# Kernel optimization log

Hardware: AMD Instinct MI355X
Metric: run time of the kernel (lower is better)

The kernel has to match this reference:

```python
import jax, jax.numpy as jnp
import numpy as np

B, N = 8, 6                 # batch, cameras
D, C = 45, 64               # depth bins, context channels
FH, FW = 8, 22              # feature-map height/width
GX, GY, GZ = 64, 64, 32     # BEV grid: W, H, D in the torch code
RES = 0.5
XOFF, YOFF, ZOFF = 16.0, 16.0, 8.0


def _frustum():
    # matches LSS.create_frustum: pixel coords over full 352x128 image, depths 1..45
    xs = jnp.linspace(0.0, 351.0, FW)
    ys = jnp.linspace(0.0, 127.0, FH)
    ds = jnp.arange(1.0, 46.0, 1.0)
    d, y, x = jnp.meshgrid(ds, ys, xs, indexing='ij')   # [D, FH, FW]
    return jnp.stack([x * d, y * d, d], axis=-1)         # [D, FH, FW, 3]


def setup_inputs() -> dict:
    key = jax.random.key(0)
    k1, k2, k3 = jax.random.split(key, 3)
    # depthNet output: softmax over depth bins
    depth = jax.nn.softmax(jax.random.normal(k1, (B, N, D, FH, FW), dtype=jnp.float32), axis=2)
    feature = jax.random.normal(k2, (B, N, C, FH, FW), dtype=jnp.float32)
    # realistic pinhole intrinsics (invertible), identity rotations, small translations
    K = jnp.array([[250.0, 0.0, 176.0], [0.0, 250.0, 64.0], [0.0, 0.0, 1.0]], dtype=jnp.float32)
    intrinsics = jnp.tile(K, (B, N, 1, 1))
    rots = jnp.tile(jnp.eye(3, dtype=jnp.float32), (B, N, 1, 1))
    trans = jax.random.normal(k3, (B, N, 3), dtype=jnp.float32) * 0.5
    return {"depth": depth, "feature": feature, "rots": rots, "trans": trans, "intrinsics": intrinsics}


def reference(depth, feature, rots, trans, intrinsics):
    fr = _frustum()                                              # [D, FH, FW, 3]
    # get_geometry: unproject frustum to world
    inv_K = jnp.linalg.inv(intrinsics)                           # [B, N, 3, 3]
    pts_c = jnp.einsum('bnij,dhwj->bndhwi', inv_K, fr)           # camera frame
    geom = jnp.einsum('bnij,bndhwj->bndhwi', rots, pts_c) + trans[:, :, None, None, None, :]

    # context = depth outer-product feature: [B, N, D, C, FH, FW] -> [B,N,D,FH,FW,C]
    ctx = (depth[:, :, :, None] * feature[:, :, None]).transpose(0, 1, 2, 4, 5, 3)
    ctx = ctx.reshape(-1, C)                                     # [P, C]
    g = geom.reshape(-1, 3)                                      # [P, 3]

    # voxel index compute (astype int truncates toward zero, matching torch .long())
    nx = ((g[:, 0] + XOFF) / RES).astype(jnp.int32)
    ny = ((g[:, 2] + YOFF) / RES).astype(jnp.int32)
    nz = ((g[:, 1] + ZOFF) / RES).astype(jnp.int32)
    valid = (nx >= 0) & (nx < GX) & (ny >= 0) & (ny < GY) & (nz >= 0) & (nz < GZ)

    bidx = jnp.repeat(jnp.arange(B, dtype=jnp.int32), N * D * FH * FW)
    idx = jnp.where(valid, bidx * (GX * GY * GZ) + nx * (GY * GZ) + ny * GZ + nz, 0)

    # scatter-sum into dense BEV grid; invalid points contribute zero
    bev = jnp.zeros((B * GX * GY * GZ, C), dtype=ctx.dtype)
    bev = bev.at[idx].add(ctx * valid[:, None].astype(ctx.dtype))
    # [B, GX, GY, GZ, C] -> [B, C, GZ, GX, GY]
    return bev.reshape(B, GX, GY, GZ, C).transpose(0, 4, 3, 1, 2)
```

## Files before the change

### kernel.cpp

```cpp
#include <hip/hip_runtime.h>

#define BB 8
#define NN 6
#define DD 45
#define CC 64
#define FHH 8
#define FWW 22
#define GXX 64
#define GYY 64
#define GZZ 32
#define NPOINTS (BB*NN*DD*FHH*FWW)
#define NSITES (BB*NN*FHH*FWW)
#define ROWS (BB*GZZ)
#define NBINS (GXX*GYY)
#define CAPR 8192
#define HWSZ (FHH*FWW)

typedef float f32x4 __attribute__((ext_vector_type(4)));

#define WS_HIST_OFF 0
#define WS_OFF_OFF  ((size_t)ROWS * NBINS * 4)
#define WS_REC_OFF  (WS_OFF_OFF + (size_t)ROWS * 4097 * 4)
#define WS_SORT_OFF (WS_REC_OFF + (size_t)NPOINTS * 4)
#define WS_FEATG_OFF (WS_SORT_OFF + (size_t)ROWS * CAPR * 8)
#define WS_CNTR_OFF (WS_FEATG_OFF + (size_t)16 * NSITES * 16)
#define WS_NEEDED (WS_CNTR_OFF + (size_t)ROWS * 4)

__device__ __forceinline__ bool geom(int p, int& row, int& nxny,
                                     const float* __restrict__ rots,
                                     const float* __restrict__ trans,
                                     const float* __restrict__ intr)
{
    int w = p % FWW;
    int t = p / FWW;
    int h = t % FHH; t /= FHH;
    int di = t % DD; t /= DD;
    int n = t % NN;
    int b = t / NN;

    float d = (float)(di + 1);
    float x = (float)(351.0 * (double)w / 21.0);
    float y = (float)(127.0 * (double)h / 7.0);

    const float* K = intr + (b * NN + n) * 9;
    double k00 = K[0], k01 = K[1], k02 = K[2];
    double k10 = K[3], k11 = K[4], k12 = K[5];
    double k20 = K[6], k21 = K[7], k22 = K[8];
    double det = k00 * (k11 * k22 - k12 * k21)
               - k01 * (k10 * k22 - k12 * k20)
               + k02 * (k10 * k21 - k11 * k20);
    double id = 1.0 / det;
    float i00 = (float)(( k11 * k22 - k12 * k21) * id);
    float i01 = (float)((-k01 * k22 + k02 * k21) * id);
    float i02 = (float)(( k01 * k12 - k02 * k11) * id);
    float i10 = (float)((-k10 * k22 + k12 * k20) * id);
    float i11 = (float)(( k00 * k22 - k02 * k20) * id);
    float i12 = (float)((-k00 * k12 + k02 * k10) * id);
    float i20 = (float)(( k10 * k21 - k11 * k20) * id);
    float i21 = (float)((-k00 * k21 + k01 * k20) * id);
    float i22 = (float)(( k00 * k11 - k01 * k10) * id);

    float p0 = x * d, p1 = y * d, p2 = d;
    float c0 = i00 * p0 + i01 * p1 + i02 * p2;
    float c1 = i10 * p0 + i11 * p1 + i12 * p2;
    float c2 = i20 * p0 + i21 * p1 + i22 * p2;

    const float* R = rots + (b * NN + n) * 9;
    const float* T = trans + (b * NN + n) * 3;
    float g0 = R[0] * c0 + R[1] * c1 + R[2] * c2 + T[0];
    float g1 = R[3] * c0 + R[4] * c1 + R[5] * c2 + T[1];
    float g2 = R[6] * c0 + R[7] * c1 + R[8] * c2 + T[2];

    int nx = (int)((g0 + 16.0f) / 0.5f);
    int ny = (int)((g2 + 16.0f) / 0.5f);
    int nz = (int)((g1 + 8.0f)  / 0.5f);
    bool valid = (nx >= 0) & (nx < GXX) & (ny >= 0) & (ny < GYY) & (nz >= 0) & (nz < GZZ);

    row  = (b * GZZ + nz);
    nxny = (nx << 6) | ny;
    return valid;
}

__global__ __launch_bounds__(256) void lss_prep(const float* __restrict__ feature,
                                                int* __restrict__ hist,
                                                float4* __restrict__ featG) {
    int i = blockIdx.x * 256 + threadIdx.x;
    int stride = gridDim.x * 256;
    int4* h4 = (int4*)hist;
    int4 z4 = make_int4(0, 0, 0, 0);
    for (int k = i; k < ROWS * NBINS / 4; k += stride) h4[k] = z4;
    for (int k = i; k < 16 * NSITES; k += stride) {
        int site = k % NSITES;
        int ccb = k / NSITES;
        int hw = site % HWSZ;
        int cam = site / HWSZ;
        const float* fb = feature + ((size_t)cam * CC + ccb * 4) * HWSZ + hw;
        featG[k] = make_float4(fb[0], fb[HWSZ], fb[2 * HWSZ], fb[3 * HWSZ]);
    }
}

__global__ __launch_bounds__(256) void lss_build1(
    const float* __restrict__ rots, const float* __restrict__ trans,
    const float* __restrict__ intr,
    int* __restrict__ rec, int* __restrict__ hist)
{
    int p = blockIdx.x * 256 + threadIdx.x;
    int row, nxny;
    if (geom(p, row, nxny, rots, trans, intr)) {
        rec[p] = (row << 12) | nxny;
        atomicAdd(&hist[row * NBINS + nxny], 1);
    } else {
        rec[p] = -1;
    }
}

__global__ __launch_bounds__(256) void lss_scan(const int* __restrict__ hist,
                                                int* __restrict__ off,
                                                int* __restrict__ cnt_row) {
    int row = blockIdx.x;
    const int* h = hist + row * NBINS;
    int* o = off + row * 4097;
    int tid = threadIdx.x;

    int vals[16]; int sum = 0;
    #pragma unroll
    for (int i = 0; i < 16; ++i) { vals[i] = sum; sum += h[tid * 16 + i]; }

    __shared__ int ts[256];
    ts[tid] = sum;
    __syncthreads();
    for (int ofs = 1; ofs < 256; ofs <<= 1) {
        int v = (tid >= ofs) ? ts[tid - ofs] : 0;
        __syncthreads();
        ts[tid] += v;
        __syncthreads();
    }
    int base = tid ? ts[tid - 1] : 0;
    #pragma unroll
    for (int i = 0; i < 16; ++i)
        o[tid * 16 + i] = base + vals[i];
    if (tid == 255) { o[4096] = ts[255]; cnt_row[row] = ts[255]; }
}

__global__ __launch_bounds__(256) void lss_build2(
    const float* __restrict__ depth, const int* __restrict__ rec,
    int* __restrict__ off, int2* __restrict__ sorted)
{
    int p = blockIdx.x * 256 + threadIdx.x;
    int r = rec[p];
    if (r < 0) return;
    int row = r >> 12;
    int nxny = r & 4095;
    int w = p % FWW;
    int t = p / FWW;
    int h = t % FHH; t /= FHH;
    int cam = t / DD;
    int site = (cam * FHH + h) * FWW + w;
    float dv = depth[p];
    int pos = atomicAdd(&off[row * 4097 + nxny], 1);
    if (pos < CAPR)
        sorted[(size_t)row * CAPR + pos] = make_int2(__float_as_int(dv), (site << 12) | nxny);
}

__global__ __launch_bounds__(256) void lss_out8(
    const float4* __restrict__ featG,
    const int* __restrict__ cnt_row,
    const int2* __restrict__ sorted,
    float* __restrict__ out)
{
    int bid = blockIdx.x;
    int ccb = bid & 15;
    int row = bid >> 4;
    int b = row >> 5, nz = row & 31;
    int tid = threadIdx.x;

    int scnt = cnt_row[row];
    if (scnt > CAPR) scnt = CAPR;

    size_t ob0 = (((size_t)b * CC + ccb * 4) * GZZ + nz) * (GXX * GYY);
    const size_t cstride = (size_t)GZZ * GXX * GYY;

    if (scnt == 0) {
        f32x4 z = (f32x4){0.f, 0.f, 0.f, 0.f};
        #pragma unroll
        for (int cc = 0; cc < 4; ++cc) {
            f32x4* op = (f32x4*)(out + ob0 + (size_t)cc * cstride);
            #pragma unroll
            for (int k = 0; k < 4; ++k) op[tid + k * 256] = z;
        }
        return;
    }

    __shared__ float acc[4 * NBINS];
    {
        f32x4 z = (f32x4){0.f, 0.f, 0.f, 0.f};
        f32x4* a4 = (f32x4*)acc;
        #pragma unroll
        for (int k = 0; k < 16; ++k) a4[tid + k * 256] = z;
    }
    __syncthreads();

    const float4* fg = featG + (size_t)ccb * NSITES;
    const int2* bk = sorted + (size_t)row * CAPR;

    int E = (scnt + 255) >> 8;
    int s0 = tid * E;
    int e0 = s0 + E; if (e0 > scnt) e0 = scnt;

    f32x4 racc = (f32x4){0.f, 0.f, 0.f, 0.f};
    int rvox = -1;
    for (int e = s0; e < e0; ++e) {
        int2 en = bk[e];
        int meta = en.y;
        int vox = meta & 4095;
        float dv = __int_as_float(en.x);
        float4 f = fg[meta >> 12];
        if (vox != rvox) {
            if (rvox >= 0) {
                atomicAdd(&acc[0 * NBINS + rvox], racc.x);
                atomicAdd(&acc[1 * NBINS + rvox], racc.y);
                atomicAdd(&acc[2 * NBINS + rvox], racc.z);
                atomicAdd(&acc[3 * NBINS + rvox], racc.w);
            }
            rvox = vox;
            racc = (f32x4){0.f, 0.f, 0.f, 0.f};
        }
        racc.x += dv * f.x;
        racc.y += dv * f.y;
        racc.z += dv * f.z;
        racc.w += dv * f.w;
    }
    if (rvox >= 0) {
        atomicAdd(&acc[0 * NBINS + rvox], racc.x);
        atomicAdd(&acc[1 * NBINS + rvox], racc.y);
        atomicAdd(&acc[2 * NBINS + rvox], racc.z);
        atomicAdd(&acc[3 * NBINS + rvox], racc.w);
    }
    __syncthreads();

    #pragma unroll
    for (int cc = 0; cc < 4; ++cc) {
        const f32x4* a4 = (const f32x4*)(acc + cc * NBINS);
        f32x4* op = (f32x4*)(out + ob0 + (size_t)cc * cstride);
        for (int i = tid; i < 1024; i += 256)
            op[i] = a4[i];
    }
}

__global__ __launch_bounds__(256) void lss_zero(float4* __restrict__ p, int n4) {
    int i = blockIdx.x * blockDim.x + threadIdx.x;
    int stride = gridDim.x * blockDim.x;
    float4 z = make_float4(0.f, 0.f, 0.f, 0.f);
    for (; i < n4; i += stride) p[i] = z;
}

__global__ __launch_bounds__(256) void lss_scatter_direct(
    const float* __restrict__ depth, const float* __restrict__ feature,
    const float* __restrict__ rots, const float* __restrict__ trans,
    const float* __restrict__ intr, float* __restrict__ out)
{
    int p = blockIdx.x * 4 + (threadIdx.x >> 6);
    int lane = threadIdx.x & 63;
    int row, nxny;
    if (!geom(p, row, nxny, rots, trans, intr)) return;
    int b = row >> 5, nz = row & 31;
    int nx = nxny >> 6, ny = nxny & 63;
    int w = p % FWW;
    int t = p / FWW;
    int h = t % FHH; t /= FHH;
    int cam = t / DD;
    float dv = depth[p];
    float fv = feature[((size_t)cam * CC + lane) * HWSZ + h * FWW + w];
    size_t oidx = ((((size_t)b * CC + lane) * GZZ + nz) * GXX + nx) * GYY + ny;
    atomicAdd(out + oidx, dv * fv);
}

extern "C" void kernel_launch(void* const* d_in, const int* in_sizes, int n_in,
                              void* d_out, int out_size, void* d_ws, size_t ws_size,
                              hipStream_t stream) {
    const float* depth   = (const float*)d_in[0];
    const float* feature = (const float*)d_in[1];
    const float* rots    = (const float*)d_in[2];
    const float* trans   = (const float*)d_in[3];
    const float* intr    = (const float*)d_in[4];
    float* out = (float*)d_out;

    if (ws_size >= WS_NEEDED) {
        int*    hist    = (int*)((char*)d_ws + WS_HIST_OFF);
        int*    off     = (int*)((char*)d_ws + WS_OFF_OFF);
        int*    rec     = (int*)((char*)d_ws + WS_REC_OFF);
        int2*   sorted  = (int2*)((char*)d_ws + WS_SORT_OFF);
        float4* featG   = (float4*)((char*)d_ws + WS_FEATG_OFF);
        int*    cnt_row = (int*)((char*)d_ws + WS_CNTR_OFF);

        lss_prep<<<1024, 256, 0, stream>>>(feature, hist, featG);
        lss_build1<<<NPOINTS / 256, 256, 0, stream>>>(rots, trans, intr, rec, hist);
        lss_scan<<<ROWS, 256, 0, stream>>>(hist, off, cnt_row);
        lss_build2<<<NPOINTS / 256, 256, 0, stream>>>(depth, rec, off, sorted);
        lss_out8<<<ROWS * 16, 256, 0, stream>>>(featG, cnt_row, sorted, out);
    } else {
        lss_zero<<<4096, 256, 0, stream>>>((float4*)out, out_size / 4);
        lss_scatter_direct<<<NPOINTS / 4, 256, 0, stream>>>(depth, feature, rots, trans, intr, out);
    }
}
```

Measured before the change: 79.46 us.

## Split output accumulation to 2 channels per block and fold feature gather into scan

Result: no change. 78.62 us (-1.1%).

```diff
diff --git a/kernel.cpp b/kernel.cpp
--- a/kernel.cpp
+++ b/kernel.cpp
@@ -17,13 +17,14 @@
 #define HWSZ (FHH*FWW)
 
 typedef float f32x4 __attribute__((ext_vector_type(4)));
+typedef float f32x2 __attribute__((ext_vector_type(2)));
 
 #define WS_HIST_OFF 0
 #define WS_OFF_OFF  ((size_t)ROWS * NBINS * 4)
 #define WS_REC_OFF  (WS_OFF_OFF + (size_t)ROWS * 4097 * 4)
 #define WS_SORT_OFF (WS_REC_OFF + (size_t)NPOINTS * 4)
 #define WS_FEATG_OFF (WS_SORT_OFF + (size_t)ROWS * CAPR * 8)
-#define WS_CNTR_OFF (WS_FEATG_OFF + (size_t)16 * NSITES * 16)
+#define WS_CNTR_OFF (WS_FEATG_OFF + (size_t)32 * NSITES * 8)
 #define WS_NEEDED (WS_CNTR_OFF + (size_t)ROWS * 4)
 
 __device__ __forceinline__ bool geom(int p, int& row, int& nxny,
@@ -81,24 +82,6 @@
     return valid;
 }
 
-__global__ __launch_bounds__(256) void lss_prep(const float* __restrict__ feature,
-                                                int* __restrict__ hist,
-                                                float4* __restrict__ featG) {
-    int i = blockIdx.x * 256 + threadIdx.x;
-    int stride = gridDim.x * 256;
-    int4* h4 = (int4*)hist;
-    int4 z4 = make_int4(0, 0, 0, 0);
-    for (int k = i; k < ROWS * NBINS / 4; k += stride) h4[k] = z4;
-    for (int k = i; k < 16 * NSITES; k += stride) {
-        int site = k % NSITES;
-        int ccb = k / NSITES;
-        int hw = site % HWSZ;
-        int cam = site / HWSZ;
-        const float* fb = feature + ((size_t)cam * CC + ccb * 4) * HWSZ + hw;
-        featG[k] = make_float4(fb[0], fb[HWSZ], fb[2 * HWSZ], fb[3 * HWSZ]);
-    }
-}
-
 __global__ __launch_bounds__(256) void lss_build1(
     const float* __restrict__ rots, const float* __restrict__ trans,
     const float* __restrict__ intr,
@@ -116,7 +99,9 @@
 
 __global__ __launch_bounds__(256) void lss_scan(const int* __restrict__ hist,
                                                 int* __restrict__ off,
-                                                int* __restrict__ cnt_row) {
+                                                int* __restrict__ cnt_row,
+                                                const float* __restrict__ feature,
+                                                float2* __restrict__ featG2) {
     int row = blockIdx.x;
     const int* h = hist + row * NBINS;
     int* o = off + row * 4097;
@@ -140,6 +125,15 @@
     for (int i = 0; i < 16; ++i)
         o[tid * 16 + i] = base + vals[i];
     if (tid == 255) { o[4096] = ts[255]; cnt_row[row] = ts[255]; }
+
+    for (int k = blockIdx.x * 256 + tid; k < 32 * NSITES; k += ROWS * 256) {
+        int site = k % NSITES;
+        int ccp = k / NSITES;
+        int hw = site % HWSZ;
+        int cam = site / HWSZ;
+        const float* fb = feature + ((size_t)cam * CC + ccp * 2) * HWSZ + hw;
+        featG2[k] = make_float2(fb[0], fb[HWSZ]);
+    }
 }
 
 __global__ __launch_bounds__(256) void lss_build2(
@@ -162,28 +156,28 @@
         sorted[(size_t)row * CAPR + pos] = make_int2(__float_as_int(dv), (site << 12) | nxny);
 }
 
-__global__ __launch_bounds__(256) void lss_out8(
-    const float4* __restrict__ featG,
+__global__ __launch_bounds__(256) void lss_out9(
+    const float2* __restrict__ featG2,
     const int* __restrict__ cnt_row,
     const int2* __restrict__ sorted,
     float* __restrict__ out)
 {
     int bid = blockIdx.x;
-    int ccb = bid & 15;
-    int row = bid >> 4;
+    int ccp = bid & 31;
+    int row = bid >> 5;
     int b = row >> 5, nz = row & 31;
     int tid = threadIdx.x;
 
     int scnt = cnt_row[row];
     if (scnt > CAPR) scnt = CAPR;
 
-    size_t ob0 = (((size_t)b * CC + ccb * 4) * GZZ + nz) * (GXX * GYY);
+    size_t ob0 = (((size_t)b * CC + ccp * 2) * GZZ + nz) * (GXX * GYY);
     const size_t cstride = (size_t)GZZ * GXX * GYY;
 
     if (scnt == 0) {
         f32x4 z = (f32x4){0.f, 0.f, 0.f, 0.f};
         #pragma unroll
-        for (int cc = 0; cc < 4; ++cc) {
+        for (int cc = 0; cc < 2; ++cc) {
             f32x4* op = (f32x4*)(out + ob0 + (size_t)cc * cstride);
             #pragma unroll
             for (int k = 0; k < 4; ++k) op[tid + k * 256] = z;
@@ -191,59 +185,54 @@
         return;
     }
 
-    __shared__ float acc[4 * NBINS];
+    __shared__ float acc[2 * NBINS];
     {
         f32x4 z = (f32x4){0.f, 0.f, 0.f, 0.f};
         f32x4* a4 = (f32x4*)acc;
         #pragma unroll
-        for (int k = 0; k < 16; ++k) a4[tid + k * 256] = z;
+        for (int k = 0; k < 8; ++k) a4[tid + k * 256] = z;
     }
     __syncthreads();
 
-    const float4* fg = featG + (size_t)ccb * NSITES;
+    const float2* fg = featG2 + (size_t)ccp * NSITES;
     const int2* bk = sorted + (size_t)row * CAPR;
 
     int E = (scnt + 255) >> 8;
     int s0 = tid * E;
     int e0 = s0 + E; if (e0 > scnt) e0 = scnt;
 
-    f32x4 racc = (f32x4){0.f, 0.f, 0.f, 0.f};
+    f32x2 racc = (f32x2){0.f, 0.f};
     int rvox = -1;
     for (int e = s0; e < e0; ++e) {
         int2 en = bk[e];
         int meta = en.y;
         int vox = meta & 4095;
         float dv = __int_as_float(en.x);
-        float4 f = fg[meta >> 12];
+        float2 f = fg[meta >> 12];
         if (vox != rvox) {
             if (rvox >= 0) {
-                atomicAdd(&acc[0 * NBINS + rvox], racc.x);
-                atomicAdd(&acc[1 * NBINS + rvox], racc.y);
-                atomicAdd(&acc[2 * NBINS + rvox], racc.z);
-                atomicAdd(&acc[3 * NBINS + rvox], racc.w);
+                atomicAdd(&acc[rvox], racc.x);
+                atomicAdd(&acc[NBINS + rvox], racc.y);
             }
             rvox = vox;
-            racc = (f32x4){0.f, 0.f, 0.f, 0.f};
+            racc = (f32x2){0.f, 0.f};
         }
         racc.x += dv * f.x;
         racc.y += dv * f.y;
-        racc.z += dv * f.z;
-        racc.w += dv * f.w;
     }
     if (rvox >= 0) {
-        atomicAdd(&acc[0 * NBINS + rvox], racc.x);
-        atomicAdd(&acc[1 * NBINS + rvox], racc.y);
-        atomicAdd(&acc[2 * NBINS + rvox], racc.z);
-        atomicAdd(&acc[3 * NBINS + rvox], racc.w);
+        atomicAdd(&acc[rvox], racc.x);
+        atomicAdd(&acc[NBINS + rvox], racc.y);
     }
     __syncthreads();
 
     #pragma unroll
-    for (int cc = 0; cc < 4; ++cc) {
+    for (int cc = 0; cc < 2; ++cc) {
         const f32x4* a4 = (const f32x4*)(acc + cc * NBINS);
         f32x4* op = (f32x4*)(out + ob0 + (size_t)cc * cstride);
-        for (int i = tid; i < 1024; i += 256)
-            op[i] = a4[i];
+        #pragma unroll
+        for (int k = 0; k < 4; ++k)
+            op[tid + k * 256] = a4[tid + k * 256];
     }
 }
 
@@ -290,14 +279,14 @@
         int*    off     = (int*)((char*)d_ws + WS_OFF_OFF);
         int*    rec     = (int*)((char*)d_ws + WS_REC_OFF);
         int2*   sorted  = (int2*)((char*)d_ws + WS_SORT_OFF);
-        float4* featG   = (float4*)((char*)d_ws + WS_FEATG_OFF);
+        float2* featG2  = (float2*)((char*)d_ws + WS_FEATG_OFF);
         int*    cnt_row = (int*)((char*)d_ws + WS_CNTR_OFF);
 
-        lss_prep<<<1024, 256, 0, stream>>>(feature, hist, featG);
+        hipMemsetAsync(hist, 0, (size_t)ROWS * NBINS * 4, stream);
         lss_build1<<<NPOINTS / 256, 256, 0, stream>>>(rots, trans, intr, rec, hist);
-        lss_scan<<<ROWS, 256, 0, stream>>>(hist, off, cnt_row);
+        lss_scan<<<ROWS, 256, 0, stream>>>(hist, off, cnt_row, feature, featG2);
         lss_build2<<<NPOINTS / 256, 256, 0, stream>>>(depth, rec, off, sorted);
-        lss_out8<<<ROWS * 16, 256, 0, stream>>>(featG, cnt_row, sorted, out);
+        lss_out9<<<ROWS * 32, 256, 0, stream>>>(featG2, cnt_row, sorted, out);
     } else {
         lss_zero<<<4096, 256, 0, stream>>>((float4*)out, out_size / 4);
         lss_scatter_direct<<<NPOINTS / 4, 256, 0, stream>>>(depth, feature, rots, trans, intr, out);
```
